# Kernel optimization log

Measured on AMD Instinct MI355X. Metric: run time of the kernel, lower is better.

Reference implementation:

```python
import jax, jax.numpy as jnp
import numpy as np

D_MODEL = 1024
N_HEADS = 16
D_KV = 64
B, S = 2, 2048


def setup_inputs() -> dict:
    key = jax.random.key(0)
    ks = jax.random.split(key, 7)
    scale = 1.0 / np.sqrt(D_MODEL)
    return {
        "query": jax.random.normal(ks[0], (B, S, D_MODEL), jnp.float32),
        "key": jax.random.normal(ks[1], (B, S, D_MODEL), jnp.float32),
        "value": jax.random.normal(ks[2], (B, S, D_MODEL), jnp.float32),
        "mask": jnp.zeros((B, 1, 1, S), jnp.float32),
        "Wq": jax.random.normal(ks[3], (D_MODEL, N_HEADS * D_KV), jnp.float32) * scale,
        "Wk": jax.random.normal(ks[4], (D_MODEL, N_HEADS * D_KV), jnp.float32) * scale,
        "Wv": jax.random.normal(ks[5], (D_MODEL, N_HEADS * D_KV), jnp.float32) * scale,
        "Wo": jax.random.normal(ks[6], (N_HEADS * D_KV, D_MODEL), jnp.float32) * scale,
    }


def _split_heads(x):
    b, s, _ = x.shape
    return x.reshape(b, s, N_HEADS, D_KV).transpose(0, 2, 1, 3)  # [B,H,S,Dk]


def reference(query, key, value, mask, Wq, Wk, Wv, Wo):
    q = _split_heads(query @ Wq)
    k = _split_heads(key @ Wk)
    v = _split_heads(value @ Wv)
    scores = jnp.einsum("bhqd,bhkd->bhqk", q, k) / jnp.sqrt(
        jnp.asarray(D_KV, scores_dtype := q.dtype)
    )
    scores = scores + mask
    attn = jax.nn.softmax(scores, axis=-1)  # dropout_rate=0 -> identity
    ctx = jnp.einsum("bhqk,bhkd->bhqd", attn, v)
    ctx = ctx.transpose(0, 2, 1, 3).reshape(query.shape[0], -1, N_HEADS * D_KV)
    hidden = ctx @ Wo
    return hidden
```

## Files before the change

kernel.cpp:

```cpp
#include <hip/hip_runtime.h>
#include <hip/hip_bf16.h>
#include <stdint.h>

typedef __bf16 bf16;
typedef __bf16 bf16x8 __attribute__((ext_vector_type(8)));
typedef __bf16 bf16x4 __attribute__((ext_vector_type(4)));
typedef float  f32x4  __attribute__((ext_vector_type(4)));
typedef float  f32x16 __attribute__((ext_vector_type(16)));

#define S_LEN  2048
#define NH     16
#define DKV    64
#define DMODEL 1024
#define LOG2E  1.4426950408889634f

#define SBAR()       __builtin_amdgcn_s_barrier()
#define SFENCE()     __builtin_amdgcn_sched_barrier(0)
#define WAIT_VM(N)   asm volatile("s_waitcnt vmcnt(" #N ")" ::: "memory")
#define WAIT_LGKM0() asm volatile("s_waitcnt lgkmcnt(0)" ::: "memory")

__device__ __forceinline__ void async_load16(const void* g, void* l) {
  __builtin_amdgcn_global_load_lds(
      (const __attribute__((address_space(1))) uint32_t*)(uintptr_t)g,
      (__attribute__((address_space(3))) uint32_t*)(uintptr_t)l,
      16, 0, 0);
}

__global__ void prep(const float* __restrict__ W0, const float* __restrict__ W1,
                     const float* __restrict__ W2, const float* __restrict__ W3,
                     const float* __restrict__ Aq, const float* __restrict__ Ak,
                     const float* __restrict__ Av,
                     bf16* __restrict__ T0, bf16* __restrict__ T1,
                     bf16* __restrict__ T2, bf16* __restrict__ T3,
                     bf16* __restrict__ Qb, bf16* __restrict__ Kb, bf16* __restrict__ Vb)
{
  const int z = blockIdx.z;
  const int tid = threadIdx.x;
  if (z < 4) {
    if (blockIdx.x >= 16) return;
    const float* W = (z == 0) ? W0 : (z == 1) ? W1 : (z == 2) ? W2 : W3;
    bf16* T = (z == 0) ? T0 : (z == 1) ? T1 : (z == 2) ? T2 : T3;
    __shared__ float tile[64][65];
    int n0 = blockIdx.x * 64, k0 = blockIdx.y * 64;
    int c4 = (tid & 15) * 4;
    int rr = tid >> 4;
    for (int g = 0; g < 4; ++g) {
      int k = g * 16 + rr;
      f32x4 v = *(const f32x4*)(W + (size_t)(k0 + k) * DMODEL + n0 + c4);
      tile[k][c4] = v[0]; tile[k][c4 + 1] = v[1];
      tile[k][c4 + 2] = v[2]; tile[k][c4 + 3] = v[3];
    }
    __syncthreads();
    int kc = tid & 7, rn2 = tid >> 3;
    for (int pass = 0; pass < 2; ++pass) {
      int rn = pass * 32 + rn2;
      bf16x8 o;
      for (int w = 0; w < 8; ++w) o[w] = (bf16)tile[kc * 8 + w][rn];
      *(bf16x8*)(T + (size_t)(n0 + rn) * DMODEL + k0 + kc * 8) = o;
    }
  } else {
    const float* S = (z == 4) ? Aq : (z == 5) ? Ak : Av;
    bf16* D = (z == 4) ? Qb : (z == 5) ? Kb : Vb;
    size_t base = (((size_t)blockIdx.y * 64 + blockIdx.x) * 256 + tid) * 16;
    f32x4 v0 = *(const f32x4*)(S + base);
    f32x4 v1 = *(const f32x4*)(S + base + 4);
    f32x4 v2 = *(const f32x4*)(S + base + 8);
    f32x4 v3 = *(const f32x4*)(S + base + 12);
    bf16x8 o0, o1;
    for (int w = 0; w < 4; ++w) { o0[w] = (bf16)v0[w]; o0[w + 4] = (bf16)v1[w]; }
    for (int w = 0; w < 4; ++w) { o1[w] = (bf16)v2[w]; o1[w + 4] = (bf16)v3[w]; }
    *(bf16x8*)(D + base) = o0;
    *(bf16x8*)(D + base + 8) = o1;
  }
}

__global__ __launch_bounds__(256) void gemm_qkv(
    const bf16* __restrict__ Aq, const bf16* __restrict__ Ak, const bf16* __restrict__ Av,
    const bf16* __restrict__ Bq, const bf16* __restrict__ Bk, const bf16* __restrict__ Bv,
    bf16* __restrict__ Cq, bf16* __restrict__ Ck, bf16* __restrict__ Cv)
{
  __shared__ __align__(16) char smem[33792];
  bf16* As = (bf16*)smem;
  bf16* Bs = (bf16*)(smem + 16384);
  bf16* Ls = (bf16*)smem;

  const int z = blockIdx.z;
  const bf16* A  = (z == 0) ? Aq : (z == 1) ? Ak : Av;
  const bf16* Bt = (z == 0) ? Bq : (z == 1) ? Bk : Bv;
  bf16* C        = (z == 0) ? Cq : (z == 1) ? Ck : Cv;

  const int m0 = blockIdx.x * 128;
  const int n0 = blockIdx.y * 128;
  const int tid = threadIdx.x;
  const int lane = tid & 63;
  const int wave = tid >> 6;
  const int wm = (wave >> 1) * 64;
  const int wn = (wave & 1) * 64;
  const int row = lane & 15;
  const int quad = lane >> 4;

  f32x4 acc[4][4];
  for (int i = 0; i < 4; ++i)
    for (int j = 0; j < 4; ++j) acc[i][j] = (f32x4){0.f, 0.f, 0.f, 0.f};

  for (int kt = 0; kt < 16; ++kt) {
    const int kk = kt << 6;
    for (int j = 0; j < 4; ++j) {
      int base = j * 256 + wave * 64;
      int idx = base + lane;
      int r = idx >> 3;
      int cc = (idx & 7) ^ (r & 7);
      async_load16(A  + (size_t)(m0 + r) * DMODEL + kk + cc * 8,
                   (char*)As + (size_t)base * 16);
      async_load16(Bt + (size_t)(n0 + r) * DMODEL + kk + cc * 8,
                   (char*)Bs + (size_t)base * 16);
    }
    WAIT_VM(0);
    SBAR();
    for (int ks = 0; ks < 2; ++ks) {
      bf16x8 af[4], bfr[4];
      for (int i = 0; i < 4; ++i) {
        int rr = wm + i * 16 + row;
        af[i] = *(const bf16x8*)(As + rr * 64 + (((quad + ks * 4) ^ (rr & 7)) << 3));
      }
      for (int j = 0; j < 4; ++j) {
        int rr = wn + j * 16 + row;
        bfr[j] = *(const bf16x8*)(Bs + rr * 64 + (((quad + ks * 4) ^ (rr & 7)) << 3));
      }
      for (int i = 0; i < 4; ++i)
        for (int j = 0; j < 4; ++j)
          acc[i][j] = __builtin_amdgcn_mfma_f32_16x16x32_bf16(af[i], bfr[j], acc[i][j], 0, 0, 0);
    }
    SBAR();
  }

  if (z != 2) {
    const int bq = m0 >> 11;
    __syncthreads();
    for (int i = 0; i < 4; ++i)
      for (int j = 0; j < 4; ++j)
        for (int r = 0; r < 4; ++r)
          Ls[(wm + i * 16 + quad * 4 + r) * 132 + wn + j * 16 + row] = (bf16)acc[i][j][r];
    __syncthreads();
    for (int u = 0; u < 8; ++u) {
      int cc = u * 256 + tid;
      int rloc = cc >> 4, c8 = (cc & 15) * 8;
      int s = (m0 + rloc) & 2047;
      int gn = n0 + c8;
      int h = gn >> 6, d = gn & 63;
      bf16x8 val = *(const bf16x8*)(Ls + rloc * 132 + c8);
      *(bf16x8*)(C + (((size_t)(bq * NH + h)) * S_LEN + s) * DKV + d) = val;
    }
  } else {
    for (int i = 0; i < 4; ++i)
      for (int j = 0; j < 4; ++j) {
        int gm = m0 + wm + i * 16 + quad * 4;
        int gn = n0 + wn + j * 16 + row;
        int b = gm >> 11, s = gm & 2047;
        int h = gn >> 6,  d = gn & 63;
        int bh = b * NH + h;
        int tile = s >> 6, kb = (s & 63) >> 2;
        int half = (kb >> 1) & 1;
        int p = (kb & 1) + ((kb >> 2) & 1) * 2 + (kb >> 3) * 4;
        bf16x4 t;
        for (int r = 0; r < 4; ++r) t[r] = (bf16)acc[i][j][r];
        *(bf16x4*)(C + ((((size_t)bh * 32 + tile) * 8 + p) * 64 + d) * 8 + half * 4) = t;
      }
  }
}

__global__ __launch_bounds__(256, 4) void attn_kernel(
    const bf16* __restrict__ Qh, const bf16* __restrict__ Kh, const bf16* __restrict__ Vperm,
    const float* __restrict__ mask, bf16* __restrict__ ctx)
{
  __shared__ __align__(16) bf16 Ks[2][64 * 64];
  __shared__ __align__(16) bf16 Vts[2][64 * 64];
  __shared__ __align__(16) float masks2[2][64];
  __shared__ float lrow[128];

  const int bh = blockIdx.x;
  const int b = bh >> 4;
  const int q0 = blockIdx.y * 128;
  const int tid = threadIdx.x;
  const int lane = tid & 63;
  const int wave = tid >> 6;
  const int ln = lane & 31;
  const int hi = lane >> 5;
  const float SC2 = 0.125f * LOG2E;

  const int qg = q0 + wave * 32 + ln;
  bf16x8 qf[4];
  {
    const bf16* qrow = Qh + ((size_t)bh * S_LEN + qg) * DKV;
    for (int c = 0; c < 4; ++c)
      qf[c] = *(const bf16x8*)(qrow + c * 16 + hi * 8);
  }

  auto stage = [&](int it, int buf) {
    const int kv0 = it * 64;
    float mval = 0.f;
    if (tid < 64) mval = mask[b * S_LEN + kv0 + tid];
    const bf16* vtile = Vperm + ((size_t)bh * 32 + it) * 4096;
    for (int j = 0; j < 2; ++j) {
      int base = j * 256 + wave * 64;
      int idx = base + lane;
      int r = idx >> 3;
      int cc = (idx & 7) ^ (r & 7);
      async_load16(Kh + ((size_t)bh * S_LEN + kv0 + r) * DKV + cc * 8,
                   (char*)Ks[buf] + (size_t)base * 16);
      async_load16(vtile + (size_t)idx * 8,
                   (char*)Vts[buf] + (size_t)base * 16);
    }
    if (tid < 64) masks2[buf][tid] = mval * LOG2E;
  };

  f32x16 O[2];
  for (int nb = 0; nb < 2; ++nb)
    for (int i = 0; i < 16; ++i) O[nb][i] = 0.f;
  float lsum = 0.f;

  stage(0, 0);

  for (int it = 0; it < 32; ++it) {
    const int cur = it & 1;
    if (it < 31) stage(it + 1, cur ^ 1);
    SFENCE();
    if (it < 31) { WAIT_VM(4); }
    else         { WAIT_VM(0); }
    WAIT_LGKM0();
    SBAR();
    SFENCE();

    f32x16 Sm[2];
    for (int i = 0; i < 16; ++i) { Sm[0][i] = 0.f; Sm[1][i] = 0.f; }
    for (int c = 0; c < 4; ++c) {
      bf16x8 k0 = *(const bf16x8*)(Ks[cur] + ln * 64        + (((2 * c + hi) ^ (ln & 7)) << 3));
      bf16x8 k1 = *(const bf16x8*)(Ks[cur] + (32 + ln) * 64 + (((2 * c + hi) ^ (ln & 7)) << 3));
      Sm[0] = __builtin_amdgcn_mfma_f32_32x32x16_bf16(k0, qf[c], Sm[0], 0, 0, 0);
      Sm[1] = __builtin_amdgcn_mfma_f32_32x32x16_bf16(k1, qf[c], Sm[1], 0, 0, 0);
    }

    for (int cg = 0; cg < 4; ++cg) {
      int mb = cg >> 1, g = cg & 1;
      int koff = 32 * mb + 16 * g + 4 * hi;
      f32x4 mklo = *(const f32x4*)(&masks2[cur][koff]);
      f32x4 mkhi = *(const f32x4*)(&masks2[cur][koff + 8]);
      bf16x8 ap;
      float ls0 = 0.f;
      for (int u = 0; u < 4; ++u) {
        float p = __builtin_amdgcn_exp2f(Sm[mb][g * 8 + u] * SC2 + mklo[u]);
        ls0 += p; ap[u] = (bf16)p;
      }
      for (int u = 0; u < 4; ++u) {
        float p = __builtin_amdgcn_exp2f(Sm[mb][g * 8 + 4 + u] * SC2 + mkhi[u]);
        ls0 += p; ap[4 + u] = (bf16)p;
      }
      lsum += ls0;
      int p = hi + 2 * g + 4 * mb;
      for (int nb = 0; nb < 2; ++nb) {
        int d = nb * 32 + ln;
        bf16x8 bv = *(const bf16x8*)(Vts[cur] + ((size_t)p * 64 + d) * 8);
        O[nb] = __builtin_amdgcn_mfma_f32_32x32x16_bf16(ap, bv, O[nb], 0, 0, 0);
      }
    }
    SFENCE();
    SBAR();
  }

  float lt = lsum + __shfl_xor(lsum, 32, 64);
  if (hi == 0) lrow[wave * 32 + ln] = 1.0f / lt;
  __syncthreads();

  const int hcol = (bh & 15) * DKV;
  for (int g = 0; g < 4; ++g)
    for (int j = 0; j < 4; ++j) {
      int qrl = wave * 32 + j + 8 * g + 4 * hi;
      float sc = lrow[qrl];
      for (int nb = 0; nb < 2; ++nb)
        ctx[((size_t)(b * S_LEN + q0 + qrl)) * DMODEL + hcol + nb * 32 + ln]
          = (bf16)(O[nb][g * 4 + j] * sc);
    }
}

__global__ __launch_bounds__(256) void gemm_out(
    const bf16* __restrict__ Ctx, const bf16* __restrict__ Wot, float* __restrict__ Cout)
{
  __shared__ __align__(16) bf16 As[2][64 * 64];
  __shared__ __align__(16) bf16 Bs[2][128 * 64];

  const int m0 = blockIdx.x * 64;
  const int n0 = blockIdx.y * 128;
  const int tid = threadIdx.x;
  const int lane = tid & 63;
  const int wave = tid >> 6;
  const int wm = (wave >> 1) * 32;
  const int wn = (wave & 1) * 64;
  const int row = lane & 15;
  const int quad = lane >> 4;

  f32x4 acc[2][4];
  for (int i = 0; i < 2; ++i)
    for (int j = 0; j < 4; ++j) acc[i][j] = (f32x4){0.f, 0.f, 0.f, 0.f};

  auto stage = [&](int kt, int buf) {
    const int kk = kt << 6;
    for (int j = 0; j < 2; ++j) {
      int base = j * 256 + wave * 64;
      int idx = base + lane;
      int r = idx >> 3;
      int cc = (idx & 7) ^ (r & 7);
      async_load16(Ctx + (size_t)(m0 + r) * DMODEL + kk + cc * 8,
                   (char*)As[buf] + (size_t)base * 16);
    }
    for (int j = 0; j < 4; ++j) {
      int base = j * 256 + wave * 64;
      int idx = base + lane;
      int r = idx >> 3;
      int cc = (idx & 7) ^ (r & 7);
      async_load16(Wot + (size_t)(n0 + r) * DMODEL + kk + cc * 8,
                   (char*)Bs[buf] + (size_t)base * 16);
    }
  };

  stage(0, 0);

  for (int kt = 0; kt < 16; ++kt) {
    const int cur = kt & 1;
    if (kt < 15) stage(kt + 1, cur ^ 1);
    SFENCE();
    if (kt < 15) { WAIT_VM(6); }
    else         { WAIT_VM(0); }
    SBAR();
    SFENCE();
    for (int ks = 0; ks < 2; ++ks) {
      bf16x8 af[2], bfr[4];
      for (int i = 0; i < 2; ++i) {
        int rr = wm + i * 16 + row;
        af[i] = *(const bf16x8*)(As[cur] + rr * 64 + (((quad + ks * 4) ^ (rr & 7)) << 3));
      }
      for (int j = 0; j < 4; ++j) {
        int rr = wn + j * 16 + row;
        bfr[j] = *(const bf16x8*)(Bs[cur] + rr * 64 + (((quad + ks * 4) ^ (rr & 7)) << 3));
      }
      for (int i = 0; i < 2; ++i)
        for (int j = 0; j < 4; ++j)
          acc[i][j] = __builtin_amdgcn_mfma_f32_16x16x32_bf16(af[i], bfr[j], acc[i][j], 0, 0, 0);
    }
    SFENCE();
    SBAR();
  }

  for (int i = 0; i < 2; ++i)
    for (int j = 0; j < 4; ++j)
      for (int r = 0; r < 4; ++r) {
        int gm = m0 + wm + i * 16 + quad * 4 + r;
        int gn = n0 + wn + j * 16 + row;
        Cout[(size_t)gm * DMODEL + gn] = acc[i][j][r];
      }
}

extern "C" void kernel_launch(void* const* d_in, const int* in_sizes, int n_in,
                              void* d_out, int out_size, void* d_ws, size_t ws_size,
                              hipStream_t stream)
{
  const float* query = (const float*)d_in[0];
  const float* key_  = (const float*)d_in[1];
  const float* value = (const float*)d_in[2];
  const float* mask  = (const float*)d_in[3];
  const float* Wq = (const float*)d_in[4];
  const float* Wk = (const float*)d_in[5];
  const float* Wv = (const float*)d_in[6];
  const float* Wo = (const float*)d_in[7];

  char* ws = (char*)d_ws;
  const size_t MB = (size_t)1 << 20;
  bf16* qh    = (bf16*)(ws + 0 * MB);
  bf16* kh    = (bf16*)(ws + 8 * MB);
  bf16* vperm = (bf16*)(ws + 16 * MB);
  bf16* wot   = (bf16*)(ws + 24 * MB);
  bf16* ctx   = (bf16*)(ws + 26 * MB);
  bf16* wqt   = (bf16*)(ws + 34 * MB);
  bf16* wkt   = (bf16*)(ws + 36 * MB);
  bf16* wvt   = (bf16*)(ws + 38 * MB);
  bf16* qb    = (bf16*)(ws + 40 * MB);
  bf16* kb    = (bf16*)(ws + 48 * MB);
  bf16* vb    = (bf16*)(ws + 56 * MB);

  prep<<<dim3(64, 16, 7), 256, 0, stream>>>(Wq, Wk, Wv, Wo, query, key_, value,
                                            wqt, wkt, wvt, wot, qb, kb, vb);
  gemm_qkv<<<dim3(32, 8, 3), 256, 0, stream>>>(qb, kb, vb, wqt, wkt, wvt,
                                               qh, kh, vperm);
  attn_kernel<<<dim3(32, 16), 256, 0, stream>>>(qh, kh, vperm, mask, ctx);
  gemm_out<<<dim3(64, 8), 256, 0, stream>>>(ctx, wot, (float*)d_out);
}
```

Before: 209.7 us.

## Split attention KV tile across wave pairs and halve query block size

Each attention block now handles 64 queries instead of 128, with four waves split into two query groups times two KV halves per tile. This doubles the grid to 1024 blocks to improve occupancy and load balance. The two KV-half partial outputs and row sums are combined through shared memory at the end, reusing the K buffer space. The cost is double the K/V tile loads per query and an extra reduction step.

```diff
diff --git a/kernel.cpp b/kernel.cpp
--- a/kernel.cpp
+++ b/kernel.cpp
@@ -173,22 +173,26 @@
     const bf16* __restrict__ Qh, const bf16* __restrict__ Kh, const bf16* __restrict__ Vperm,
     const float* __restrict__ mask, bf16* __restrict__ ctx)
 {
-  __shared__ __align__(16) bf16 Ks[2][64 * 64];
-  __shared__ __align__(16) bf16 Vts[2][64 * 64];
-  __shared__ __align__(16) float masks2[2][64];
-  __shared__ float lrow[128];
+  __shared__ __align__(16) char smem[33792];
+  bf16* Ks0 = (bf16*)smem;
+  bf16* Vts0 = (bf16*)(smem + 16384);
+  float* masks2 = (float*)(smem + 32768);
+  float* lpart  = (float*)(smem + 33280);
+  float* Of     = (float*)smem;
 
   const int bh = blockIdx.x;
   const int b = bh >> 4;
-  const int q0 = blockIdx.y * 128;
+  const int q0 = blockIdx.y * 64;
   const int tid = threadIdx.x;
   const int lane = tid & 63;
   const int wave = tid >> 6;
+  const int qi = wave & 1;
+  const int mi = wave >> 1;
   const int ln = lane & 31;
   const int hi = lane >> 5;
   const float SC2 = 0.125f * LOG2E;
 
-  const int qg = q0 + wave * 32 + ln;
+  const int qg = q0 + qi * 32 + ln;
   bf16x8 qf[4];
   {
     const bf16* qrow = Qh + ((size_t)bh * S_LEN + qg) * DKV;
@@ -207,11 +211,11 @@
       int r = idx >> 3;
       int cc = (idx & 7) ^ (r & 7);
       async_load16(Kh + ((size_t)bh * S_LEN + kv0 + r) * DKV + cc * 8,
-                   (char*)Ks[buf] + (size_t)base * 16);
+                   (char*)(Ks0 + buf * 4096) + (size_t)base * 16);
       async_load16(vtile + (size_t)idx * 8,
-                   (char*)Vts[buf] + (size_t)base * 16);
-    }
-    if (tid < 64) masks2[buf][tid] = mval * LOG2E;
+                   (char*)(Vts0 + buf * 4096) + (size_t)base * 16);
+    }
+    if (tid < 64) masks2[buf * 64 + tid] = mval * LOG2E;
   };
 
   f32x16 O[2];
@@ -231,35 +235,39 @@
     SBAR();
     SFENCE();
 
-    f32x16 Sm[2];
-    for (int i = 0; i < 16; ++i) { Sm[0][i] = 0.f; Sm[1][i] = 0.f; }
-    for (int c = 0; c < 4; ++c) {
-      bf16x8 k0 = *(const bf16x8*)(Ks[cur] + ln * 64        + (((2 * c + hi) ^ (ln & 7)) << 3));
-      bf16x8 k1 = *(const bf16x8*)(Ks[cur] + (32 + ln) * 64 + (((2 * c + hi) ^ (ln & 7)) << 3));
-      Sm[0] = __builtin_amdgcn_mfma_f32_32x32x16_bf16(k0, qf[c], Sm[0], 0, 0, 0);
-      Sm[1] = __builtin_amdgcn_mfma_f32_32x32x16_bf16(k1, qf[c], Sm[1], 0, 0, 0);
-    }
-
-    for (int cg = 0; cg < 4; ++cg) {
-      int mb = cg >> 1, g = cg & 1;
-      int koff = 32 * mb + 16 * g + 4 * hi;
-      f32x4 mklo = *(const f32x4*)(&masks2[cur][koff]);
-      f32x4 mkhi = *(const f32x4*)(&masks2[cur][koff + 8]);
+    const bf16* Ksc = Ks0 + cur * 4096;
+    const bf16* Vtc = Vts0 + cur * 4096;
+    const float* mks = masks2 + cur * 64;
+
+    f32x16 Sm;
+    for (int i = 0; i < 16; ++i) Sm[i] = 0.f;
+    {
+      const int rr = mi * 32 + ln;
+      for (int c = 0; c < 4; ++c) {
+        bf16x8 k0 = *(const bf16x8*)(Ksc + rr * 64 + (((2 * c + hi) ^ (ln & 7)) << 3));
+        Sm = __builtin_amdgcn_mfma_f32_32x32x16_bf16(k0, qf[c], Sm, 0, 0, 0);
+      }
+    }
+
+    for (int g = 0; g < 2; ++g) {
+      int koff = mi * 32 + 16 * g + 4 * hi;
+      f32x4 mklo = *(const f32x4*)(mks + koff);
+      f32x4 mkhi = *(const f32x4*)(mks + koff + 8);
       bf16x8 ap;
       float ls0 = 0.f;
       for (int u = 0; u < 4; ++u) {
-        float p = __builtin_amdgcn_exp2f(Sm[mb][g * 8 + u] * SC2 + mklo[u]);
+        float p = __builtin_amdgcn_exp2f(Sm[g * 8 + u] * SC2 + mklo[u]);
         ls0 += p; ap[u] = (bf16)p;
       }
       for (int u = 0; u < 4; ++u) {
-        float p = __builtin_amdgcn_exp2f(Sm[mb][g * 8 + 4 + u] * SC2 + mkhi[u]);
+        float p = __builtin_amdgcn_exp2f(Sm[g * 8 + 4 + u] * SC2 + mkhi[u]);
         ls0 += p; ap[4 + u] = (bf16)p;
       }
       lsum += ls0;
-      int p = hi + 2 * g + 4 * mb;
+      int p = hi + 2 * g + 4 * mi;
       for (int nb = 0; nb < 2; ++nb) {
         int d = nb * 32 + ln;
-        bf16x8 bv = *(const bf16x8*)(Vts[cur] + ((size_t)p * 64 + d) * 8);
+        bf16x8 bv = *(const bf16x8*)(Vtc + ((size_t)p * 64 + d) * 8);
         O[nb] = __builtin_amdgcn_mfma_f32_32x32x16_bf16(ap, bv, O[nb], 0, 0, 0);
       }
     }
@@ -268,18 +276,31 @@
   }
 
   float lt = lsum + __shfl_xor(lsum, 32, 64);
-  if (hi == 0) lrow[wave * 32 + ln] = 1.0f / lt;
+  if (hi == 0) lpart[mi * 64 + qi * 32 + ln] = lt;
+
+  if (mi == 1) {
+    for (int g = 0; g < 4; ++g)
+      for (int j = 0; j < 4; ++j) {
+        int qrl = qi * 32 + j + 8 * g + 4 * hi;
+        for (int nb = 0; nb < 2; ++nb)
+          Of[qrl * 64 + nb * 32 + ln] = O[nb][g * 4 + j];
+      }
+  }
   __syncthreads();
 
-  const int hcol = (bh & 15) * DKV;
-  for (int g = 0; g < 4; ++g)
-    for (int j = 0; j < 4; ++j) {
-      int qrl = wave * 32 + j + 8 * g + 4 * hi;
-      float sc = lrow[qrl];
-      for (int nb = 0; nb < 2; ++nb)
-        ctx[((size_t)(b * S_LEN + q0 + qrl)) * DMODEL + hcol + nb * 32 + ln]
-          = (bf16)(O[nb][g * 4 + j] * sc);
-    }
+  if (mi == 0) {
+    const int hcol = (bh & 15) * DKV;
+    for (int g = 0; g < 4; ++g)
+      for (int j = 0; j < 4; ++j) {
+        int qrl = qi * 32 + j + 8 * g + 4 * hi;
+        float sc = 1.0f / (lpart[qrl] + lpart[64 + qrl]);
+        for (int nb = 0; nb < 2; ++nb) {
+          float v = O[nb][g * 4 + j] + Of[qrl * 64 + nb * 32 + ln];
+          ctx[((size_t)(b * S_LEN + q0 + qrl)) * DMODEL + hcol + nb * 32 + ln]
+            = (bf16)(v * sc);
+        }
+      }
+  }
 }
 
 __global__ __launch_bounds__(256) void gemm_out(
@@ -390,6 +411,6 @@
                                             wqt, wkt, wvt, wot, qb, kb, vb);
   gemm_qkv<<<dim3(32, 8, 3), 256, 0, stream>>>(qb, kb, vb, wqt, wkt, wvt,
                                                qh, kh, vperm);
-  attn_kernel<<<dim3(32, 16), 256, 0, stream>>>(qh, kh, vperm, mask, ctx);
+  attn_kernel<<<dim3(32, 32), 256, 0, stream>>>(qh, kh, vperm, mask, ctx);
   gemm_out<<<dim3(64, 8), 256, 0, stream>>>(ctx, wot, (float*)d_out);
 }
```

Measured after the change: 214.8 us. 1.02x slower.
